# Optimization experiments

Hardware: AMD Instinct MI355X
Metric: run time of the kernel (lower is better)

Reference implementation:

```python
import jax, jax.numpy as jnp
import numpy as np

N = 50000
F = 256
E = 800000


def setup_inputs() -> dict:
    key = jax.random.key(0)
    k1, k2, k3, k4 = jax.random.split(key, 4)
    H = jax.random.normal(k1, (N, F), dtype=jnp.float32)
    H0 = jax.random.normal(k2, (N, F), dtype=jnp.float32)
    # edge list for sparse adjacency: row 0 = i (row index), row 1 = j (col index)
    edge_index = jax.random.randint(k3, (2, E), 0, N, dtype=jnp.int32)
    # W ~ U(-stdv, stdv), stdv = 1/sqrt(out_features), as in reset_parameters
    stdv = 1.0 / np.sqrt(F)
    W = jax.random.uniform(k4, (F, F), minval=-stdv, maxval=stdv, dtype=jnp.float32)
    lamda = jnp.float32(0.5)
    alpha = jnp.float32(0.1)
    l = 4
    return {"H": H, "edge_index": edge_index, "H0": H0, "W": W,
            "lamda": lamda, "alpha": alpha, "l": l}


def reference(H, edge_index, H0, W, lamda, alpha, l):
    n = H.shape[0]
    src = edge_index[0]  # i: row index of A[i, j]
    dst = edge_index[1]  # j: col index
    # A_hat = A + I ; degree = column sums of A_hat (tf.reduce_sum(A_hat, 0))
    deg = jax.ops.segment_sum(jnp.ones(src.shape[0], dtype=H.dtype), dst,
                              num_segments=n) + 1.0
    d_inv_sqrt = jax.lax.rsqrt(deg)
    # (P H)_i = d_i^{-1/2} * sum_j A[i,j] d_j^{-1/2} H_j  +  H_i / d_i  (self loop)
    msg = H[dst] * d_inv_sqrt[dst][:, None]            # [E, F]
    agg = jax.ops.segment_sum(msg, src, num_segments=n)  # [N, F]
    PH = d_inv_sqrt[:, None] * agg + H / deg[:, None]
    init_res = (1.0 - alpha) * PH + alpha * H0
    beta = jnp.log(lamda / l + 1.0)
    # init_res @ ((1-beta) I + beta W)
    output = (1.0 - beta) * init_res + beta * (init_res @ W)
    return output
```

## Files before the change

### kernel.cpp

```cpp
#include <hip/hip_runtime.h>
#include <math.h>


#define F_DIM 256
#define CHUNK 20000

typedef __attribute__((ext_vector_type(4))) float f32x4;
typedef __attribute__((ext_vector_type(8))) short short8;
typedef __attribute__((ext_vector_type(4))) unsigned short u16x4;

static __device__ __forceinline__ unsigned short f2bf(float f) {
    unsigned int u = __float_as_uint(f);
    u += 0x7fffu + ((u >> 16) & 1u);
    return (unsigned short)(u >> 16);
}
static __device__ __forceinline__ float bf2f(unsigned short u) {
    return __uint_as_float((unsigned int)u << 16);
}


__global__ __launch_bounds__(1024) void hist_kernel(
        const int* __restrict__ src, const int* __restrict__ dst,
        unsigned* __restrict__ histS, unsigned* __restrict__ histD,
        unsigned short* __restrict__ lrank, int E, int wpc, int whalf) {
    __shared__ unsigned hist[12544];
    int b = blockIdx.x;
    int which = b & 1, h = (b >> 1) & 1, c = b >> 2;
    int tid = threadIdx.x;
    int w0 = h * whalf;
    int hcount = h ? (wpc - whalf) : whalf;
    int e0 = c * CHUNK;
    int e1 = e0 + CHUNK < E ? e0 + CHUNK : E;
    const int* eptr = which ? dst : src;
    unsigned* outh = which ? histD : histS;

    for (int w = tid; w < hcount; w += 1024) hist[w] = 0;
    __syncthreads();
    for (int e = e0 + tid; e < e1; e += 1024) {
        int s = eptr[e];
        int wl = (s >> 1) - w0;
        if ((unsigned)wl < (unsigned)hcount) {
            int sh = (s & 1) * 16;
            unsigned old = atomicAdd(&hist[wl], 1u << sh);
            if (!which) lrank[e] = (unsigned short)((old >> sh) & 0xffffu);
        }
    }
    __syncthreads();
    for (int w = tid; w < hcount; w += 1024)
        outh[(size_t)c * wpc + w0 + w] = hist[w];
}


__global__ __launch_bounds__(256) void sumbase_kernel(
        const unsigned* __restrict__ histS, const unsigned* __restrict__ histD,
        int* __restrict__ cnt, float* __restrict__ dinv,
        unsigned* __restrict__ baseL, int* __restrict__ blksum,
        int wpc, int nchunk, int n) {
    int tid = threadIdx.x;
    int w = blockIdx.x * 256 + tid;
    unsigned slo = 0, shi = 0, dlo = 0, dhi = 0;
    if (w < wpc) {
        for (int c = 0; c < nchunk; ++c) {
            unsigned vs = histS[(size_t)c * wpc + w];
            unsigned vd = histD[(size_t)c * wpc + w];
            baseL[(size_t)c * wpc + w] = slo | (shi << 16);
            slo += vs & 0xffffu; shi += vs >> 16;
            dlo += vd & 0xffffu; dhi += vd >> 16;
        }
        int i0 = 2 * w, i1 = 2 * w + 1;
        cnt[i0] = (int)slo;
        dinv[i0] = rsqrtf((float)dlo + 1.0f);
        if (i1 < n) {
            cnt[i1] = (int)shi;
            dinv[i1] = rsqrtf((float)dhi + 1.0f);
        }
    }
    int contrib = 0;
    if (w < wpc) {
        contrib = (int)slo;
        if (2 * w + 1 < n) contrib += (int)shi;
    }
    int lane = tid & 63, wid = tid >> 6;
    int v = contrib;
    for (int off = 32; off > 0; off >>= 1) v += __shfl_down(v, off, 64);
    __shared__ int ws4[4];
    if (lane == 0) ws4[wid] = v;
    __syncthreads();
    if (tid == 0)   blksum[2 * blockIdx.x]     = ws4[0] + ws4[1];
    if (tid == 128) blksum[2 * blockIdx.x + 1] = ws4[2] + ws4[3];
}


__global__ __launch_bounds__(256) void rowptr_kernel(const int* __restrict__ cnt,
                                                     const int* __restrict__ blksum,
                                                     int* __restrict__ row_ptr,
                                                     int n, int nb) {
    int tid = threadIdx.x;
    int lane = tid & 63, w = tid >> 6;
    int bv = (tid < nb) ? blksum[tid] : 0;
    int bs = bv;
    for (int off = 1; off < 64; off <<= 1) {
        int t = __shfl_up(bv, off, 64);
        if (lane >= off) bv += t;
    }
    __shared__ int wsb[4];
    __shared__ int sbo[256];
    if (lane == 63) wsb[w] = bv;
    __syncthreads();
    if (tid == 0) {
        int run = 0;
        for (int k = 0; k < 4; ++k) { int t = wsb[k]; wsb[k] = run; run += t; }
    }
    __syncthreads();
    sbo[tid] = wsb[w] + bv - bs;
    __syncthreads();
    int blockoff = sbo[blockIdx.x];
    int i = blockIdx.x * 256 + tid;
    int s = (i < n) ? cnt[i] : 0;
    int v = s;
    for (int off = 1; off < 64; off <<= 1) {
        int t = __shfl_up(v, off, 64);
        if (lane >= off) v += t;
    }
    __shared__ int ws[4];
    if (lane == 63) ws[w] = v;
    __syncthreads();
    if (tid == 0) {
        int run = 0;
        for (int k = 0; k < 4; ++k) { int t = ws[k]; ws[k] = run; run += t; }
    }
    __syncthreads();
    if (i <= n) row_ptr[i] = blockoff + ws[w] + v - s;
}


__global__ __launch_bounds__(256) void fillhswt_kernel(
        const int* __restrict__ src, const int* __restrict__ dst,
        const int* __restrict__ row_ptr, const unsigned* __restrict__ baseL,
        const unsigned short* __restrict__ lrank, int* __restrict__ col,
        const float* __restrict__ H, const float* __restrict__ dinv,
        unsigned short* __restrict__ Hs,
        const float* __restrict__ W, unsigned short* __restrict__ Wt,
        const float* __restrict__ lamda_p, const int* __restrict__ l_p,
        int E, int wpc, int nfill, int total4) {
    int bid = blockIdx.x;
    int tid = threadIdx.x;
    if (bid < nfill) {
        int e = bid * 256 + tid;
        if (e < E) {
            int c = e / CHUNK;
            int s = src[e];
            unsigned word = baseL[(size_t)c * wpc + (s >> 1)];
            unsigned lb = (s & 1) ? (word >> 16) : (word & 0xffffu);
            unsigned pos = (unsigned)row_ptr[s] + lb + lrank[e];
            col[pos] = dst[e];
        }
    } else {
        int i = (bid - nfill) * 256 + tid;
        if (i < total4) {
            int row = i >> 6;
            float d = dinv[row];
            f32x4 x = ((const f32x4*)H)[i];
            u16x4 o;
            o[0] = f2bf(x[0] * d); o[1] = f2bf(x[1] * d);
            o[2] = f2bf(x[2] * d); o[3] = f2bf(x[3] * d);
            ((u16x4*)Hs)[i] = o;
        } else {
            int t = i - total4;
            if (t < F_DIM * F_DIM) {
                float beta = logf(lamda_p[0] / (float)l_p[0] + 1.0f);
                int nn = t >> 8, kk = t & 255;
                float v = beta * W[kk * F_DIM + nn];
                if (kk == nn) v += 1.0f - beta;
                Wt[nn * F_DIM + kk] = f2bf(v);
            }
        }
    }
}


#define ACC(A, h) { A[0] += bf2f(h[0]); A[1] += bf2f(h[1]); \
                    A[2] += bf2f(h[2]); A[3] += bf2f(h[3]); }

__global__ __launch_bounds__(256) void gather_kernel(
        const unsigned short* __restrict__ Hs, const float* __restrict__ H0,
        const int* __restrict__ row_ptr, const int* __restrict__ col,
        const float* __restrict__ dinv, const float* __restrict__ alpha_p,
        unsigned short* __restrict__ irb, int n) {
    int wave = threadIdx.x >> 6;
    int lane = threadIdx.x & 63;
    int row = blockIdx.x * 4 + wave;
    if (row >= n) return;
    float alpha = alpha_p[0];
    const u16x4* Hs4 = (const u16x4*)Hs;

    int beg = row_ptr[row], end = row_ptr[row + 1];
    f32x4 a0 = 0.0f, a1 = 0.0f, a2 = 0.0f, a3 = 0.0f;
    int e = beg;
    for (; e + 8 <= end; e += 8) {
        int j0 = col[e+0], j1 = col[e+1], j2 = col[e+2], j3 = col[e+3];
        int j4 = col[e+4], j5 = col[e+5], j6 = col[e+6], j7 = col[e+7];
        u16x4 h0 = Hs4[j0*64+lane], h1 = Hs4[j1*64+lane];
        u16x4 h2 = Hs4[j2*64+lane], h3 = Hs4[j3*64+lane];
        u16x4 h4 = Hs4[j4*64+lane], h5 = Hs4[j5*64+lane];
        u16x4 h6 = Hs4[j6*64+lane], h7 = Hs4[j7*64+lane];
        ACC(a0, h0) ACC(a1, h1) ACC(a2, h2) ACC(a3, h3)
        ACC(a0, h4) ACC(a1, h5) ACC(a2, h6) ACC(a3, h7)
    }
    for (; e + 4 <= end; e += 4) {
        int j0 = col[e+0], j1 = col[e+1], j2 = col[e+2], j3 = col[e+3];
        u16x4 h0 = Hs4[j0*64+lane], h1 = Hs4[j1*64+lane];
        u16x4 h2 = Hs4[j2*64+lane], h3 = Hs4[j3*64+lane];
        ACC(a0, h0) ACC(a1, h1) ACC(a2, h2) ACC(a3, h3)
    }
    for (; e < end; ++e) {
        int j = col[e];
        u16x4 h = Hs4[j*64+lane];
        ACC(a0, h)
    }
    u16x4 hr = Hs4[row*64+lane];
    ACC(a2, hr)
    f32x4 acc = (a0 + a1) + (a2 + a3);
    float di = dinv[row];
    f32x4 h0v = __builtin_nontemporal_load((const f32x4*)H0 + row * 64 + lane);
    f32x4 init = (1.0f - alpha) * (di * acc) + alpha * h0v;
    u16x4 o;
    o[0] = f2bf(init[0]); o[1] = f2bf(init[1]);
    o[2] = f2bf(init[2]); o[3] = f2bf(init[3]);
    __builtin_nontemporal_store(o, (u16x4*)irb + row * 64 + lane);
}


__global__ __launch_bounds__(256) void gemm_kernel(
        const unsigned short* __restrict__ irb, const unsigned short* __restrict__ Wt,
        float* __restrict__ out, int M) {
    int w = threadIdx.x >> 6;
    int mr = blockIdx.x * 64;
    int nc = w * 64;
    int lane = threadIdx.x & 63;
    int lo = lane & 15, hi = lane >> 4;

    f32x4 acc[4][4] = {};
    for (int kk = 0; kk < 8; ++kk) {
        int kb = kk * 32 + hi * 8;
        short8 a[4], b[4];
        for (int am = 0; am < 4; ++am) {
            int row = mr + am * 16 + lo;
            a[am] = (row < M) ? *(const short8*)(irb + (size_t)row * F_DIM + kb)
                              : (short8)0;
        }
        for (int bn = 0; bn < 4; ++bn) {
            int cb = nc + bn * 16 + lo;
            b[bn] = *(const short8*)(Wt + cb * F_DIM + kb);
        }
        for (int am = 0; am < 4; ++am)
            for (int bn = 0; bn < 4; ++bn)
                acc[am][bn] = __builtin_amdgcn_mfma_f32_16x16x32_bf16(
                    a[am], b[bn], acc[am][bn], 0, 0, 0);
    }

    for (int am = 0; am < 4; ++am) {
        int rbase = mr + am * 16 + hi * 4;
        for (int r = 0; r < 4; ++r) {
            int row = rbase + r;
            if (row >= M) continue;
            for (int bn = 0; bn < 4; ++bn) {
                int c2 = nc + bn * 16 + lo;
                out[(size_t)row * F_DIM + c2] = acc[am][bn][r];
            }
        }
    }
}


extern "C" void kernel_launch(void* const* d_in, const int* in_sizes, int n_in,
                              void* d_out, int out_size, void* d_ws, size_t ws_size,
                              hipStream_t stream) {
    const float* H     = (const float*)d_in[0];
    const int*   ei    = (const int*)d_in[1];
    const float* H0    = (const float*)d_in[2];
    const float* W     = (const float*)d_in[3];
    const float* lamda = (const float*)d_in[4];
    const float* alpha = (const float*)d_in[5];
    const int*   lp    = (const int*)d_in[6];

    int n = in_sizes[0] / F_DIM;
    int E = in_sizes[1] / 2;
    const int* src = ei;
    const int* dst = ei + E;
    float* out = (float*)d_out;

    int wpc = (n + 1) / 2;
    int whalf = (wpc + 1) / 2;
    int nchunk = (E + CHUNK - 1) / CHUNK;
    int nb = (n + 256) / 256;

    char* ws = (char*)d_ws;
    size_t off = 0;
    auto alloc = [&](size_t bytes) -> void* {
        void* p = ws + off;
        off += (bytes + 255) & ~(size_t)255;
        return p;
    };
    unsigned* histS = (unsigned*)alloc((size_t)nchunk * wpc * 4);
    unsigned* histD = (unsigned*)alloc((size_t)nchunk * wpc * 4);
    unsigned* baseL = (unsigned*)alloc((size_t)nchunk * wpc * 4);
    unsigned short* lrank = (unsigned short*)alloc((size_t)E * 2);
    int* cnt     = (int*)alloc((size_t)n * 4);
    int* row_ptr = (int*)alloc(((size_t)n + 1) * 4);
    int* blksum  = (int*)alloc((size_t)(nb + 8) * 4);
    float* dinv  = (float*)alloc((size_t)n * 4);
    int* colb    = (int*)alloc((size_t)E * 4);
    unsigned short* Wt  = (unsigned short*)alloc((size_t)F_DIM * F_DIM * 2);
    unsigned short* Hs  = (unsigned short*)alloc((size_t)n * F_DIM * 2);
    unsigned short* irb = (unsigned short*)alloc(((size_t)n + 64) * F_DIM * 2);

    hist_kernel<<<nchunk * 4, 1024, 0, stream>>>(src, dst, histS, histD, lrank,
                                                 E, wpc, whalf);
    int wgrid = (wpc + 255) / 256;
    sumbase_kernel<<<wgrid, 256, 0, stream>>>(histS, histD, cnt, dinv, baseL,
                                              blksum, wpc, nchunk, n);
    rowptr_kernel<<<nb, 256, 0, stream>>>(cnt, blksum, row_ptr, n, nb);
    int nfill = (E + 255) / 256;
    int total4 = n * 64;
    int nhswt = (total4 + F_DIM * F_DIM + 255) / 256;
    fillhswt_kernel<<<nfill + nhswt, 256, 0, stream>>>(
        src, dst, row_ptr, baseL, lrank, colb,
        H, dinv, Hs, W, Wt, lamda, lp, E, wpc, nfill, total4);
    gather_kernel<<<(n + 3) / 4, 256, 0, stream>>>(Hs, H0, row_ptr, colb, dinv,
                                                   alpha, irb, n);
    int mtiles = (n + 63) / 64;
    gemm_kernel<<<mtiles, 256, 0, stream>>>(irb, Wt, out, n);
}
```

Measured before the change: 165.7 us.

## Pack per-chunk histogram counters into 8-bit lanes to fit one LDS pass

Degree histogram counters are packed four per 32-bit word with 8-bit fields instead of two per word with 16-bit fields. The whole node range then fits in shared memory, so each edge chunk is processed by one block instead of two half-range blocks that each rescanned the chunk. The local-rank and base-offset arrays become bytes, which shrinks the memory traffic in the hist, sumbase and fill kernels, and the sumbase block sums are now written per wave. The cost is that any node appearing more than 255 times in a 20000-edge chunk would overflow into its neighbour's byte. With uniform random edges that is very unlikely, but it is not guaranteed in general.

```diff
diff --git a/kernel.cpp b/kernel.cpp
--- a/kernel.cpp
+++ b/kernel.cpp
@@ -22,32 +22,27 @@
 __global__ __launch_bounds__(1024) void hist_kernel(
         const int* __restrict__ src, const int* __restrict__ dst,
         unsigned* __restrict__ histS, unsigned* __restrict__ histD,
-        unsigned short* __restrict__ lrank, int E, int wpc, int whalf) {
+        unsigned char* __restrict__ lrank, int E, int wpc4) {
     __shared__ unsigned hist[12544];
     int b = blockIdx.x;
-    int which = b & 1, h = (b >> 1) & 1, c = b >> 2;
+    int which = b & 1, c = b >> 1;
     int tid = threadIdx.x;
-    int w0 = h * whalf;
-    int hcount = h ? (wpc - whalf) : whalf;
     int e0 = c * CHUNK;
     int e1 = e0 + CHUNK < E ? e0 + CHUNK : E;
     const int* eptr = which ? dst : src;
     unsigned* outh = which ? histD : histS;
 
-    for (int w = tid; w < hcount; w += 1024) hist[w] = 0;
+    for (int w = tid; w < wpc4; w += 1024) hist[w] = 0;
     __syncthreads();
     for (int e = e0 + tid; e < e1; e += 1024) {
         int s = eptr[e];
-        int wl = (s >> 1) - w0;
-        if ((unsigned)wl < (unsigned)hcount) {
-            int sh = (s & 1) * 16;
-            unsigned old = atomicAdd(&hist[wl], 1u << sh);
-            if (!which) lrank[e] = (unsigned short)((old >> sh) & 0xffffu);
-        }
-    }
-    __syncthreads();
-    for (int w = tid; w < hcount; w += 1024)
-        outh[(size_t)c * wpc + w0 + w] = hist[w];
+        int sh = (s & 3) * 8;
+        unsigned old = atomicAdd(&hist[s >> 2], 1u << sh);
+        if (!which) lrank[e] = (unsigned char)((old >> sh) & 0xffu);
+    }
+    __syncthreads();
+    for (int w = tid; w < wpc4; w += 1024)
+        outh[(size_t)c * wpc4 + w] = hist[w];
 }
 
 
@@ -55,39 +50,36 @@
         const unsigned* __restrict__ histS, const unsigned* __restrict__ histD,
         int* __restrict__ cnt, float* __restrict__ dinv,
         unsigned* __restrict__ baseL, int* __restrict__ blksum,
-        int wpc, int nchunk, int n) {
+        int wpc4, int nchunk, int n) {
     int tid = threadIdx.x;
     int w = blockIdx.x * 256 + tid;
-    unsigned slo = 0, shi = 0, dlo = 0, dhi = 0;
-    if (w < wpc) {
+    unsigned s0 = 0, s1 = 0, s2 = 0, s3 = 0;
+    unsigned d0 = 0, d1 = 0, d2 = 0, d3 = 0;
+    if (w < wpc4) {
         for (int c = 0; c < nchunk; ++c) {
-            unsigned vs = histS[(size_t)c * wpc + w];
-            unsigned vd = histD[(size_t)c * wpc + w];
-            baseL[(size_t)c * wpc + w] = slo | (shi << 16);
-            slo += vs & 0xffffu; shi += vs >> 16;
-            dlo += vd & 0xffffu; dhi += vd >> 16;
-        }
-        int i0 = 2 * w, i1 = 2 * w + 1;
-        cnt[i0] = (int)slo;
-        dinv[i0] = rsqrtf((float)dlo + 1.0f);
-        if (i1 < n) {
-            cnt[i1] = (int)shi;
-            dinv[i1] = rsqrtf((float)dhi + 1.0f);
-        }
-    }
-    int contrib = 0;
-    if (w < wpc) {
-        contrib = (int)slo;
-        if (2 * w + 1 < n) contrib += (int)shi;
-    }
+            unsigned vs = histS[(size_t)c * wpc4 + w];
+            unsigned vd = histD[(size_t)c * wpc4 + w];
+            baseL[(size_t)c * wpc4 + w] = s0 | (s1 << 8) | (s2 << 16) | (s3 << 24);
+            s0 += vs & 0xffu; s1 += (vs >> 8) & 0xffu;
+            s2 += (vs >> 16) & 0xffu; s3 += vs >> 24;
+            d0 += vd & 0xffu; d1 += (vd >> 8) & 0xffu;
+            d2 += (vd >> 16) & 0xffu; d3 += vd >> 24;
+        }
+        int i0 = 4 * w;
+        unsigned sv[4] = {s0, s1, s2, s3};
+        unsigned dv[4] = {d0, d1, d2, d3};
+        for (int k = 0; k < 4; ++k) {
+            if (i0 + k < n) {
+                cnt[i0 + k] = (int)sv[k];
+                dinv[i0 + k] = rsqrtf((float)dv[k] + 1.0f);
+            }
+        }
+    }
+    int contrib = (w < wpc4) ? (int)(s0 + s1 + s2 + s3) : 0;
     int lane = tid & 63, wid = tid >> 6;
     int v = contrib;
     for (int off = 32; off > 0; off >>= 1) v += __shfl_down(v, off, 64);
-    __shared__ int ws4[4];
-    if (lane == 0) ws4[wid] = v;
-    __syncthreads();
-    if (tid == 0)   blksum[2 * blockIdx.x]     = ws4[0] + ws4[1];
-    if (tid == 128) blksum[2 * blockIdx.x + 1] = ws4[2] + ws4[3];
+    if (lane == 0) blksum[4 * blockIdx.x + wid] = v;
 }
 
 
@@ -136,13 +128,13 @@
 
 __global__ __launch_bounds__(256) void fillhswt_kernel(
         const int* __restrict__ src, const int* __restrict__ dst,
-        const int* __restrict__ row_ptr, const unsigned* __restrict__ baseL,
-        const unsigned short* __restrict__ lrank, int* __restrict__ col,
+        const int* __restrict__ row_ptr, const unsigned char* __restrict__ baseL8,
+        const unsigned char* __restrict__ lrank, int* __restrict__ col,
         const float* __restrict__ H, const float* __restrict__ dinv,
         unsigned short* __restrict__ Hs,
         const float* __restrict__ W, unsigned short* __restrict__ Wt,
         const float* __restrict__ lamda_p, const int* __restrict__ l_p,
-        int E, int wpc, int nfill, int total4) {
+        int E, int wpc4, int nfill, int total4) {
     int bid = blockIdx.x;
     int tid = threadIdx.x;
     if (bid < nfill) {
@@ -150,8 +142,7 @@
         if (e < E) {
             int c = e / CHUNK;
             int s = src[e];
-            unsigned word = baseL[(size_t)c * wpc + (s >> 1)];
-            unsigned lb = (s & 1) ? (word >> 16) : (word & 0xffffu);
+            unsigned lb = baseL8[(size_t)c * (4 * wpc4) + s];
             unsigned pos = (unsigned)row_ptr[s] + lb + lrank[e];
             col[pos] = dst[e];
         }
@@ -290,8 +281,7 @@
     const int* dst = ei + E;
     float* out = (float*)d_out;
 
-    int wpc = (n + 1) / 2;
-    int whalf = (wpc + 1) / 2;
+    int wpc4 = (n + 3) / 4;
     int nchunk = (E + CHUNK - 1) / CHUNK;
     int nb = (n + 256) / 256;
 
@@ -302,10 +292,10 @@
         off += (bytes + 255) & ~(size_t)255;
         return p;
     };
-    unsigned* histS = (unsigned*)alloc((size_t)nchunk * wpc * 4);
-    unsigned* histD = (unsigned*)alloc((size_t)nchunk * wpc * 4);
-    unsigned* baseL = (unsigned*)alloc((size_t)nchunk * wpc * 4);
-    unsigned short* lrank = (unsigned short*)alloc((size_t)E * 2);
+    unsigned* histS = (unsigned*)alloc((size_t)nchunk * wpc4 * 4);
+    unsigned* histD = (unsigned*)alloc((size_t)nchunk * wpc4 * 4);
+    unsigned* baseL = (unsigned*)alloc((size_t)nchunk * wpc4 * 4);
+    unsigned char* lrank = (unsigned char*)alloc((size_t)E);
     int* cnt     = (int*)alloc((size_t)n * 4);
     int* row_ptr = (int*)alloc(((size_t)n + 1) * 4);
     int* blksum  = (int*)alloc((size_t)(nb + 8) * 4);
@@ -315,18 +305,18 @@
     unsigned short* Hs  = (unsigned short*)alloc((size_t)n * F_DIM * 2);
     unsigned short* irb = (unsigned short*)alloc(((size_t)n + 64) * F_DIM * 2);
 
-    hist_kernel<<<nchunk * 4, 1024, 0, stream>>>(src, dst, histS, histD, lrank,
-                                                 E, wpc, whalf);
-    int wgrid = (wpc + 255) / 256;
+    hist_kernel<<<nchunk * 2, 1024, 0, stream>>>(src, dst, histS, histD, lrank,
+                                                 E, wpc4);
+    int wgrid = (wpc4 + 255) / 256;
     sumbase_kernel<<<wgrid, 256, 0, stream>>>(histS, histD, cnt, dinv, baseL,
-                                              blksum, wpc, nchunk, n);
+                                              blksum, wpc4, nchunk, n);
     rowptr_kernel<<<nb, 256, 0, stream>>>(cnt, blksum, row_ptr, n, nb);
     int nfill = (E + 255) / 256;
     int total4 = n * 64;
     int nhswt = (total4 + F_DIM * F_DIM + 255) / 256;
     fillhswt_kernel<<<nfill + nhswt, 256, 0, stream>>>(
-        src, dst, row_ptr, baseL, lrank, colb,
-        H, dinv, Hs, W, Wt, lamda, lp, E, wpc, nfill, total4);
+        src, dst, row_ptr, (const unsigned char*)baseL, lrank, colb,
+        H, dinv, Hs, W, Wt, lamda, lp, E, wpc4, nfill, total4);
     gather_kernel<<<(n + 3) / 4, 256, 0, stream>>>(Hs, H0, row_ptr, colb, dinv,
                                                    alpha, irb, n);
     int mtiles = (n + 63) / 64;
```

Result: no change. 165.9 us (+0.1%).
